# Performance work log

Measured on AMD Instinct MI355X. Metric: run time of the kernel, lower is better.

The kernel has to match this reference:

```python
import jax, jax.numpy as jnp
from jax import lax
import numpy as np

B, S, E, HID = 16, 7, 64, 64
RES = (64, 64); D = RES[0] * RES[1]
XLOW, XHIGH = -0.5, 0.5
RLOW, RHIGH = float(np.sqrt(0.01)), float(np.sqrt(0.05))
PIXEL_MULT = 1.0; N_ITER = 3; TSOFT = 1.0 / float(np.sqrt(E))

def _build_grid():
    ranges = [np.linspace(XLOW, XHIGH, r) for r in RES]
    g = np.stack(np.meshgrid(*ranges, indexing='xy'), axis=-1)
    g = g.reshape(RES[0], RES[1], -1).reshape(1, -1, 2)
    return jnp.asarray(g, dtype=jnp.float32)

ABS_GRID = _build_grid()  # [1, D, 2]

def _ln(x, g, b):
    m = jnp.mean(x, -1, keepdims=True)
    v = jnp.mean(jnp.square(x - m), -1, keepdims=True)
    return (x - m) * lax.rsqrt(v + 1e-5) * g + b

def _forward(data, slot_noise, pos_rand, conv0_w, conv0_b, conv1_w, conv1_b, conv2_w, conv2_b,
             dataN_g, dataN_b, queryN_g, queryN_b, toK_w, toK_b, toV_w, toV_b, dense_w, dense_b,
             mlp1_w, mlp1_b, mlp2_w, mlp2_b, gru_wih, gru_whh, gru_bih, gru_bhh,
             alpha1_w, alpha1_b, alpha2_w, alpha2_b, final1_w, final1_b, final2_w, final2_b,
             slots_mu, slots_logsigma):
    dn = ('NCHW', 'OIHW', 'NCHW')
    def conv(x, w, b):
        return lax.conv_general_dilated(x, w, (1, 1), 'SAME', dimension_numbers=dn) + b[None, :, None, None]
    # CNN encoder: Conv-ReLU x3, 'same' padding, k=5
    x = jax.nn.relu(conv(data, conv0_w, conv0_b))
    x = jax.nn.relu(conv(x, conv1_w, conv1_b))
    x = jax.nn.relu(conv(x, conv2_w, conv2_b))
    enc = x.transpose(0, 2, 3, 1).reshape(B, D, HID)
    enc = _ln(enc, dataN_g, dataN_b)

    queries = slots_mu + jnp.exp(slots_logsigma) * slot_noise  # [B,S,E]
    # init_slots: faithful replication (source indexes the SLOT dim, and swaps rlow/rhigh)
    pos_scale = pos_rand.at[:, :2, :].add(-0.5)
    pos_scale = pos_scale.at[:, -1, :].set((RLOW - RHIGH) * pos_rand[:, -1, :] + RHIGH)

    encK = enc @ toK_w + toK_b  # [B,D,E]
    encV = enc @ toV_w + toV_b

    def init_mlp(y):
        y = _ln(y, queryN_g, queryN_b)
        return jax.nn.relu(y @ mlp1_w + mlp1_b) @ mlp2_w + mlp2_b

    def get_kv(ps):
        # per-slot relative grid: [B,S,D,2]
        rel = (ABS_GRID[:, None] - ps[:, :, None, :2]) / ps[:, :, -1][:, :, None, None]
        eg = PIXEL_MULT * (rel @ dense_w + dense_b)  # [B,S,D,E]
        return init_mlp(encK[:, None] + eg), init_mlp(encV[:, None] + eg)

    def att_wts(q, k):
        logits = jnp.einsum('bse,bsde->bsd', q, k) * TSOFT
        att = jax.nn.softmax(logits, axis=1)  # softmax over slots
        wts = att / jnp.sum(att, -1, keepdims=True) + 1e-8
        return att, wts

    def update_frames(wts):
        new_pos = jnp.einsum('bsd,de->bse', wts, ABS_GRID[0])  # [B,S,2]
        d2 = jnp.sum(jnp.square(ABS_GRID[:, None] - new_pos[:, :, None]), -1)  # [B,S,D]
        new_scale = jnp.sqrt(jnp.einsum('bsd,bsd->bs', wts, d2))
        return jnp.concatenate([new_pos, new_scale[..., None]], -1)

    def gru(xg, h):
        gi = xg @ gru_wih.T + gru_bih
        gh = h @ gru_whh.T + gru_bhh
        ir, iz, inn = jnp.split(gi, 3, -1)
        hr, hz, hn = jnp.split(gh, 3, -1)
        r = jax.nn.sigmoid(ir + hr)
        z = jax.nn.sigmoid(iz + hz)
        n = jnp.tanh(inn + r * hn)
        return (1.0 - z) * n + z * h

    for _ in range(N_ITER):
        keys, vals = get_kv(pos_scale)
        att, wts = att_wts(_ln(queries, queryN_g, queryN_b), keys)
        pos_scale = update_frames(wts)
        upd = jnp.einsum('bsd,bsde->bse', wts, vals)
        queries = gru(upd.reshape(-1, E), queries.reshape(-1, E)).reshape(B, S, E)

    keys, _ = get_kv(pos_scale)
    att, wts = att_wts(_ln(queries, queryN_g, queryN_b), keys)
    nps = update_frames(wts)
    alpha = jax.nn.sigmoid(jax.nn.relu(queries @ alpha1_w + alpha1_b) @ alpha2_w + alpha2_b)
    slot_feat = jax.nn.relu(queries @ final1_w + final1_b) @ final2_w + final2_b + nps
    return queries, att, slot_feat, alpha

def setup_inputs() -> dict:
    ks = jax.random.split(jax.random.key(0), 20)
    f32 = jnp.float32
    def rn(i, shape, s):
        return jax.random.normal(ks[i], shape, f32) * s
    inp = dict(
        data=jax.random.normal(ks[0], (B, 1, RES[0], RES[1]), f32),
        slot_noise=jax.random.normal(ks[1], (B, S, E), f32),
        pos_rand=jax.random.uniform(ks[2], (B, S, 3), dtype=f32),
        conv0_w=rn(3, (HID, 1, 5, 5), 0.2), conv0_b=jnp.zeros(HID, f32),
        conv1_w=rn(4, (HID, HID, 5, 5), 0.025), conv1_b=jnp.zeros(HID, f32),
        conv2_w=rn(5, (HID, HID, 5, 5), 0.025), conv2_b=jnp.zeros(HID, f32),
        dataN_g=jnp.ones(HID, f32), dataN_b=jnp.zeros(HID, f32),
        queryN_g=jnp.ones(E, f32), queryN_b=jnp.zeros(E, f32),
        toK_w=rn(6, (HID, E), 0.125), toK_b=jnp.zeros(E, f32),
        toV_w=rn(7, (HID, E), 0.125), toV_b=jnp.zeros(E, f32),
        dense_w=rn(8, (2, E), 0.7), dense_b=jnp.zeros(E, f32),
        mlp1_w=rn(9, (E, E), 0.125), mlp1_b=jnp.zeros(E, f32),
        mlp2_w=rn(10, (E, E), 0.125), mlp2_b=jnp.zeros(E, f32),
        gru_wih=rn(11, (3 * E, E), 0.125), gru_whh=rn(12, (3 * E, E), 0.125),
        gru_bih=jnp.zeros(3 * E, f32), gru_bhh=jnp.zeros(3 * E, f32),
        alpha1_w=rn(13, (E, 32), 0.125), alpha1_b=jnp.zeros(32, f32),
        alpha2_w=rn(14, (32, 1), 0.18), alpha2_b=jnp.zeros(1, f32),
        final1_w=rn(15, (E, HID), 0.125), final1_b=jnp.zeros(HID, f32),
        final2_w=rn(16, (HID, 3), 0.125), final2_b=jnp.zeros(3, f32),
        slots_mu=rn(17, (1, 1, E), 1.0),
        slots_logsigma=rn(18, (1, 1, E), 0.01),
    )
    return inp

def reference(data, slot_noise, pos_rand, conv0_w, conv0_b, conv1_w, conv1_b, conv2_w, conv2_b,
              dataN_g, dataN_b, queryN_g, queryN_b, toK_w, toK_b, toV_w, toV_b, dense_w, dense_b,
              mlp1_w, mlp1_b, mlp2_w, mlp2_b, gru_wih, gru_whh, gru_bih, gru_bhh,
              alpha1_w, alpha1_b, alpha2_w, alpha2_b, final1_w, final1_b, final2_w, final2_b,
              slots_mu, slots_logsigma):
    return _forward(data, slot_noise, pos_rand, conv0_w, conv0_b, conv1_w, conv1_b, conv2_w, conv2_b,
                    dataN_g, dataN_b, queryN_g, queryN_b, toK_w, toK_b, toV_w, toV_b, dense_w, dense_b,
                    mlp1_w, mlp1_b, mlp2_w, mlp2_b, gru_wih, gru_whh, gru_bih, gru_bhh,
                    alpha1_w, alpha1_b, alpha2_w, alpha2_b, final1_w, final1_b, final2_w, final2_b,
                    slots_mu, slots_logsigma)
```

## Files before the change

kernel.cpp:

```cpp
#include <hip/hip_runtime.h>
#include <cmath>


#define RLOW_F 0.1f
#define RHIGH_F 0.22360679774997896f
#define W0CONST 1.00004096f
#define SR2 704.3386243f

typedef __attribute__((ext_vector_type(8))) __bf16 bf16x8;
typedef __attribute__((ext_vector_type(4))) float f32x4;

__device__ __forceinline__ float wsum64(float v){
  #pragma unroll
  for (int off = 32; off > 0; off >>= 1) v += __shfl_xor(v, off, 64);
  return v;
}
__device__ __forceinline__ float rdlane(float v, int l){
  return __int_as_float(__builtin_amdgcn_readlane(__float_as_int(v), l));
}
__device__ __forceinline__ unsigned short bf16bits(float v){
  __bf16 h = (__bf16)v;
  return *reinterpret_cast<unsigned short*>(&h);
}

__device__ __forceinline__ void pp_core(int row, int e, float qv,
    float px, float py, float sc,
    const float* __restrict__ qg_, const float* __restrict__ qb_,
    const float* __restrict__ dw, const float* __restrict__ db,
    const float* __restrict__ mlp2w, const float* __restrict__ mlp2b,
    float* __restrict__ absc, float* __restrict__ w2qc){
  float m = wsum64(qv) * (1.f/64.f);
  float d = qv - m;
  float var = wsum64(d*d) * (1.f/64.f);
  float qlnv = d * (1.0f/sqrtf(var + 1e-5f)) * qg_[e] + qb_[e];
  float A  = dw[e]      / sc;
  float Bv = dw[64 + e] / sc;
  absc[row*192 + e]       = A;
  absc[row*192 + 64 + e]  = Bv;
  absc[row*192 + 128 + e] = db[e] - px*A - py*Bv;
  float acc = 0.f;
  const float* wrow = mlp2w + e*64;
  for (int j = 0; j < 64; j++) acc = fmaf(wrow[j], rdlane(qlnv, j), acc);
  w2qc[row*68 + e] = acc;
  float c2 = wsum64(mlp2b[e] * qlnv);
  if (e == 0) w2qc[row*68 + 64] = c2;
}

__global__ void k_prep(const float* __restrict__ noise, const float* __restrict__ prand,
                       const float* __restrict__ mu, const float* __restrict__ logsig,
                       const float* __restrict__ qg_, const float* __restrict__ qb_,
                       const float* __restrict__ dw, const float* __restrict__ db,
                       const float* __restrict__ mlp2w, const float* __restrict__ mlp2b,
                       float* __restrict__ queries, float* __restrict__ ps,
                       float* __restrict__ absc, float* __restrict__ w2qc,
                       float* __restrict__ accF, float* __restrict__ upd){
  int row = blockIdx.x;
  int e = threadIdx.x;
  int s = row % 7;
  float qv = mu[e] + expf(logsig[e]) * noise[row*64 + e];
  queries[row*64 + e] = qv;
  upd[row*64 + e] = 0.f;
  if (e < 4) accF[row*4 + e] = 0.f;
  float pv = 0.f;
  if (e < 3){
    float pr = prand[row*3 + e];
    if (s < 2)       pv = pr - 0.5f;
    else if (s == 6) pv = (RLOW_F - RHIGH_F)*pr + RHIGH_F;
    else             pv = pr;
    ps[row*3 + e] = pv;
  }
  float px = rdlane(pv, 0), py = rdlane(pv, 1), sc = rdlane(pv, 2);
  pp_core(row, e, qv, px, py, sc, qg_, qb_, dw, db, mlp2w, mlp2b, absc, w2qc);
}

__global__ __launch_bounds__(256) void k_conv0(const float* __restrict__ in,
                        const float* __restrict__ w, const float* __restrict__ bias,
                        unsigned short* __restrict__ out){
  int bi = blockIdx.x; int b = bi >> 6; int y = bi & 63;
  int t = threadIdx.x; int lane = t & 63; int xg = t >> 6;
  __shared__ float s_in[5*68];
  __shared__ float s_w[64*25];
  __shared__ float s_out[64*65];
  for (int i = t; i < 1600; i += 256) s_w[i] = w[i];
  for (int i = t; i < 340; i += 256){
    int r = i / 68, cx = i % 68;
    int yy = y + r - 2, gx = cx - 2;
    float v = 0.f;
    if (yy >= 0 && yy < 64 && gx >= 0 && gx < 64) v = in[(b*64 + yy)*64 + gx];
    s_in[r*68 + cx] = v;
  }
  __syncthreads();
  int o = lane;
  float bvv = bias[o];
  float acc[16];
  #pragma unroll
  for (int k = 0; k < 16; k++) acc[k] = bvv;
  #pragma unroll
  for (int ky = 0; ky < 5; ky++){
    float rv[20];
    const float4* p = reinterpret_cast<const float4*>(&s_in[ky*68 + xg*16]);
    #pragma unroll
    for (int q = 0; q < 5; q++){ float4 f = p[q]; rv[q*4]=f.x; rv[q*4+1]=f.y; rv[q*4+2]=f.z; rv[q*4+3]=f.w; }
    #pragma unroll
    for (int kx = 0; kx < 5; kx++){
      float wv = s_w[o*25 + ky*5 + kx];
      #pragma unroll
      for (int k = 0; k < 16; k++) acc[k] = fmaf(rv[k+kx], wv, acc[k]);
    }
  }
  #pragma unroll
  for (int k = 0; k < 16; k++) s_out[o*65 + xg*16 + k] = fmaxf(acc[k], 0.f);
  __syncthreads();
  for (int i = t; i < 4096; i += 256){
    int px = i >> 6, ch = i & 63;
    out[((size_t)(b*64 + y)*64 + px)*64 + ch] = bf16bits(s_out[ch*65 + px]);
  }
}

__global__ void k_packconv(const float* __restrict__ w, unsigned short* __restrict__ out){
  int idx = blockIdx.x*256 + threadIdx.x;
  if (idx >= 102400) return;
  int j = idx & 7;
  int l = (idx >> 3) & 63;
  int frag = idx >> 9;
  int nt = frag & 3;
  int ks = (frag >> 2) % 10;
  int dy = frag / 40;
  int q = l >> 4, cr = l & 15;
  int k = ks*32 + q*8 + j;
  int kx = k >> 6, ch = k & 63;
  int n = nt*16 + cr;
  out[idx] = bf16bits(w[((n*64 + ch)*5 + dy)*5 + kx]);
}

__global__ __launch_bounds__(256) void k_convm(const unsigned short* __restrict__ in_bf,
                        const unsigned short* __restrict__ wpack,
                        const float* __restrict__ bias,
                        const float* __restrict__ lng, const float* __restrict__ lnb,
                        unsigned short* __restrict__ out_bf, int mode){
  int bi = blockIdx.x;
  int b = bi >> 5; int yg = (bi >> 1) & 15; int xh = bi & 1;
  int t = threadIdx.x; int wv = t >> 6; int l = t & 63;
  int q = l >> 4, cr = l & 15;
  int yr = wv >> 1, ph = wv & 1;
  int p0 = ph*16;

  __shared__ char lds[8*36*144];

  for (int ri = 0; ri < 8; ri++){
    int yy = yg*4 + ri - 2;
    bool rok = (yy >= 0 && yy < 64);
    const uint4* src = reinterpret_cast<const uint4*>(in_bf + (size_t)(b*64 + yy)*64*64);
    for (int i = t; i < 288; i += 256){
      int px = i >> 3, c8 = i & 7;
      uint4 v = {0u,0u,0u,0u};
      int gx = xh*32 + px - 2;
      if (rok && gx >= 0 && gx < 64) v = src[gx*8 + c8];
// ... 54 lines not shown
      #pragma unroll
      for (int reg = 0; reg < 4; reg++){
        int p = xh*32 + p0 + q*4 + reg;
        float v[4]; float s1 = 0.f, s2 = 0.f;
        #pragma unroll
        for (int nt = 0; nt < 4; nt++){
          v[nt] = fmaxf(acc[r][nt][reg] + bvv[nt], 0.f);
          s1 += v[nt]; s2 += v[nt]*v[nt];
        }
        #pragma unroll
        for (int m = 1; m < 16; m <<= 1){ s1 += __shfl_xor(s1, m, 64); s2 += __shfl_xor(s2, m, 64); }
        float mean = s1 * (1.f/64.f);
        float var  = s2 * (1.f/64.f) - mean*mean;
        float rstd = 1.0f/sqrtf(var + 1e-5f);
        size_t base = ((size_t)b*4096 + y*64 + p)*64;
        #pragma unroll
        for (int nt = 0; nt < 4; nt++)
          out_bf[base + nt*16 + cr] = bf16bits((v[nt] - mean)*rstd*gv[nt] + bb[nt]);
      }
    }
  }
}

__global__ void k_packw1(const float* __restrict__ w1, unsigned short* __restrict__ out){
  int idx = blockIdx.x*256 + threadIdx.x;
  int jj = idx & 7;
  int lane = (idx >> 3) & 63;
  int frag = idx >> 9;
  int ks = frag >> 2, nt = frag & 3;
  int q = lane >> 4, cr = lane & 15;
  int k = ks*32 + q*8 + jj;
  int n = nt*16 + cr;
  out[idx] = bf16bits(w1[k*64 + n]);
}

__global__ __launch_bounds__(256) void k_projm(const unsigned short* __restrict__ enc,
                       const unsigned short* __restrict__ kpack, const float* __restrict__ bk,
                       const unsigned short* __restrict__ vpack, const float* __restrict__ bvp,
                       unsigned short* __restrict__ K, unsigned short* __restrict__ V){
  int bi = blockIdx.x; int b = bi >> 6; int tile = bi & 63;
  int t = threadIdx.x; int wv = t >> 6; int l = t & 63;
  int q = l >> 4, cr = l & 15;
  int d0 = tile*64 + wv*16;

  const bf16x8* kp = reinterpret_cast<const bf16x8*>(kpack);
  const bf16x8* vp = reinterpret_cast<const bf16x8*>(vpack);
  bf16x8 KB[8], VB[8];
  #pragma unroll
  for (int f = 0; f < 8; f++){ KB[f] = kp[f*64 + l]; VB[f] = vp[f*64 + l]; }

  const unsigned short* er = enc + (size_t)(b*4096 + d0 + cr)*64;
  bf16x8 a0 = *reinterpret_cast<const bf16x8*>(er + q*8);
  bf16x8 a1 = *reinterpret_cast<const bf16x8*>(er + 32 + q*8);

  f32x4 zero = {0.f,0.f,0.f,0.f};
  f32x4 aK[4], aV[4];
  #pragma unroll
  for (int nt = 0; nt < 4; nt++){
    aK[nt] = __builtin_amdgcn_mfma_f32_16x16x32_bf16(a0, KB[nt],     zero,   0, 0, 0);
    aK[nt] = __builtin_amdgcn_mfma_f32_16x16x32_bf16(a1, KB[4 + nt], aK[nt], 0, 0, 0);
    aV[nt] = __builtin_amdgcn_mfma_f32_16x16x32_bf16(a0, VB[nt],     zero,   0, 0, 0);
    aV[nt] = __builtin_amdgcn_mfma_f32_16x16x32_bf16(a1, VB[4 + nt], aV[nt], 0, 0, 0);
  }
  #pragma unroll
  for (int nt = 0; nt < 4; nt++){
    float bkv = bk[nt*16 + cr], bvv = bvp[nt*16 + cr];
    #pragma unroll
    for (int reg = 0; reg < 4; reg++){
      size_t base = ((size_t)b*4096 + d0 + q*4 + reg)*64 + nt*16 + cr;
      K[base] = bf16bits(aK[nt][reg] + bkv);
      V[base] = bf16bits(aV[nt][reg] + bvv);
    }
  }
}

__global__ __launch_bounds__(256) void k_attnK(const unsigned short* __restrict__ encX,
     const unsigned short* __restrict__ w1pack, const float* __restrict__ mlp1b,
     const float* __restrict__ absc, const float* __restrict__ qg_,
     const float* __restrict__ qb_, const float* __restrict__ w2qc,
     float* __restrict__ att, float* __restrict__ accF){
  int bi = blockIdx.x;
  int b = bi >> 6, tile = bi & 63;
  int t = threadIdx.x; int wv = t >> 6; int l = t & 63;
  int q = l >> 4, cr = l & 15;
  int m0 = tile*64 + wv*16;
  int drow = m0 + cr;

  __shared__ float s_log[7*64];
  __shared__ float s_absc[7*192];
  __shared__ float s_wq[7*68];
  __shared__ unsigned short s_w1[4096];
  for (int i = t; i < 1344; i += 256) s_absc[i] = absc[b*7*192 + i];
  for (int i = t; i < 476;  i += 256) s_wq[i]   = w2qc[b*7*68 + i];
  {
    const uint4* g = reinterpret_cast<const uint4*>(w1pack);
    uint4* d = reinterpret_cast<uint4*>(s_w1);
    for (int i = t; i < 512; i += 256) d[i] = g[i];
  }

  const unsigned short* er = encX + (size_t)(b*4096 + drow)*64;
  float gx = -0.5f + (float)(drow & 63) * (1.f/63.f);
  float gy = -0.5f + (float)((drow >> 6) & 63) * (1.f/63.f);
  float xb[16], gq[16], bq[16];
  {
    bf16x8 ea = *reinterpret_cast<const bf16x8*>(er + q*8);
    bf16x8 eb = *reinterpret_cast<const bf16x8*>(er + 32 + q*8);
    #pragma unroll
    for (int i = 0; i < 8; i++){ xb[i] = (float)ea[i]; xb[8+i] = (float)eb[i]; }
  }
  #pragma unroll
  for (int h = 0; h < 2; h++){
    int fb = h ? (32 + q*8) : (q*8);
    const float4* g4 = reinterpret_cast<const float4*>(qg_ + fb);
    const float4* b4 = reinterpret_cast<const float4*>(qb_ + fb);
    #pragma unroll
    for (int p = 0; p < 2; p++){
      float4 gg = g4[p], bb = b4[p];
      int o = h*8 + p*4;
      gq[o+0]=gg.x; gq[o+1]=gg.y; gq[o+2]=gg.z; gq[o+3]=gg.w;
      bq[o+0]=bb.x; bq[o+1]=bb.y; bq[o+2]=bb.z; bq[o+3]=bb.w;
    }
  }
  float b1v[4];
  #pragma unroll
  for (int nt = 0; nt < 4; nt++) b1v[nt] = mlp1b[nt*16 + cr];
  __syncthreads();

  const bf16x8* wl = reinterpret_cast<const bf16x8*>(s_w1);
  f32x4 zero = {0.f, 0.f, 0.f, 0.f};

  for (int sp = 0; sp < 4; sp++){
// ... 99 lines not shown
      for (int reg = 0; reg < 4; reg++){
        s_log[s0*64 + wv*16 + q*4 + reg] = (p0[reg] + c20) * 0.125f;
        if (np == 2) s_log[sB*64 + wv*16 + q*4 + reg] = (p1[reg] + c21) * 0.125f;
      }
    }
  }
  __syncthreads();

  if (t < 64){
    float lv[7];
    #pragma unroll
    for (int s = 0; s < 7; s++) lv[s] = s_log[s*64 + t];
    float mx = lv[0];
    #pragma unroll
    for (int s = 1; s < 7; s++) mx = fmaxf(mx, lv[s]);
    float sm = 0.f;
    #pragma unroll
    for (int s = 0; s < 7; s++){ lv[s] = expf(lv[s] - mx); sm += lv[s]; }
    float inv = 1.0f / sm;
    #pragma unroll
    for (int s = 0; s < 7; s++){
      float a = lv[s] * inv;
      s_log[s*64 + t] = a;
      att[(size_t)(b*7+s)*4096 + tile*64 + t] = a;
    }
  }
  __syncthreads();

  if (t < 224){
    int s = t >> 5, r = t & 31;
    float a1 = s_log[s*64 + r];
    float a2 = s_log[s*64 + r + 32];
    float gx1 = -0.5f + (float)r * (1.f/63.f);
    float gx2 = -0.5f + (float)(r + 32) * (1.f/63.f);
    float gyc = -0.5f + (float)tile * (1.f/63.f);
    float gy2c = gyc*gyc;
    float w0 = a1 + a2;
    float w1 = a1*gx1 + a2*gx2;
    float w2 = w0*gyc;
    float w3 = a1*(gx1*gx1 + gy2c) + a2*(gx2*gx2 + gy2c);
    #pragma unroll
    for (int m = 1; m < 32; m <<= 1){
      w0 += __shfl_xor(w0, m, 64);
      w1 += __shfl_xor(w1, m, 64);
      w2 += __shfl_xor(w2, m, 64);
      w3 += __shfl_xor(w3, m, 64);
    }
    if (r == 0){
      atomicAdd(&accF[(b*7+s)*4 + 0], w0);
      atomicAdd(&accF[(b*7+s)*4 + 1], w1);
      atomicAdd(&accF[(b*7+s)*4 + 2], w2);
      atomicAdd(&accF[(b*7+s)*4 + 3], w3);
    }
  }
}

__global__ __launch_bounds__(256) void k_attnV(const unsigned short* __restrict__ encX,
     const unsigned short* __restrict__ w1pack, const float* __restrict__ mlp1b,
     const float* __restrict__ absc, const float* __restrict__ qg_,
     const float* __restrict__ qb_, const float* __restrict__ att,
     const float* __restrict__ accF, float* __restrict__ upd){
  int bi = blockIdx.x;
  int b = bi >> 6, tile = bi & 63;
  int t = threadIdx.x; int wv = t >> 6; int l = t & 63;
  int q = l >> 4, cr = l & 15;
  int m0 = tile*64 + wv*16;
  int drow = m0 + cr;

  __shared__ float s_absc[7*192];
  __shared__ float s_att[7*64];
  __shared__ float s_upd[7*64];
  __shared__ float s_inv[7];
  __shared__ unsigned short s_w1[4096];
  for (int i = t; i < 1344; i += 256) s_absc[i] = absc[b*7*192 + i];
  for (int i = t; i < 448;  i += 256){
    s_att[i] = att[(size_t)(b*7 + (i >> 6))*4096 + tile*64 + (i & 63)];
    s_upd[i] = 0.f;
  }
  if (t < 7) s_inv[t] = 1.0f / accF[(b*7 + t)*4];
  {
    const uint4* g = reinterpret_cast<const uint4*>(w1pack);
    uint4* d = reinterpret_cast<uint4*>(s_w1);
    for (int i = t; i < 512; i += 256) d[i] = g[i];
  }

  const unsigned short* er = encX + (size_t)(b*4096 + drow)*64;
  float gx = -0.5f + (float)(drow & 63) * (1.f/63.f);
  float gy = -0.5f + (float)((drow >> 6) & 63) * (1.f/63.f);
  float xb[16], gq[16], bq[16];
  {
    bf16x8 ea = *reinterpret_cast<const bf16x8*>(er + q*8);
    bf16x8 eb = *reinterpret_cast<const bf16x8*>(er + 32 + q*8);
    #pragma unroll
    for (int i = 0; i < 8; i++){ xb[i] = (float)ea[i]; xb[8+i] = (float)eb[i]; }
  }
  #pragma unroll
  for (int h = 0; h < 2; h++){
    int fb = h ? (32 + q*8) : (q*8);
    const float4* g4 = reinterpret_cast<const float4*>(qg_ + fb);
    const float4* b4 = reinterpret_cast<const float4*>(qb_ + fb);
    #pragma unroll
    for (int p = 0; p < 2; p++){
      float4 gg = g4[p], bb = b4[p];
      int o = h*8 + p*4;
      gq[o+0]=gg.x; gq[o+1]=gg.y; gq[o+2]=gg.z; gq[o+3]=gg.w;
      bq[o+0]=bb.x; bq[o+1]=bb.y; bq[o+2]=bb.z; bq[o+3]=bb.w;
    }
  }
  float b1v[4];
  #pragma unroll
  for (int nt = 0; nt < 4; nt++) b1v[nt] = mlp1b[nt*16 + cr];
  __syncthreads();

  const bf16x8* wl = reinterpret_cast<const bf16x8*>(s_w1);
  f32x4 zero = {0.f, 0.f, 0.f, 0.f};

  for (int sp = 0; sp < 4; sp++){
    int s0 = sp*2;
    int np = (sp == 3) ? 1 : 2;
    int sB = (np == 2) ? s0 + 1 : s0;
    float x0[16], x1[16];
    float s1a = 0.f, s2a = 0.f, s1b = 0.f, s2b = 0.f;
    {
      const float* Ac = s_absc + s0*192;
      #pragma unroll
      for (int h = 0; h < 2; h++){
        int fb = h ? (32 + q*8) : (q*8);
        const float4* A4 = reinterpret_cast<const float4*>(Ac + fb);
        const float4* B4 = reinterpret_cast<const float4*>(Ac + 64 + fb);
        const float4* C4 = reinterpret_cast<const float4*>(Ac + 128 + fb);
        #pragma unroll
        for (int p = 0; p < 2; p++){
          float4 Av = A4[p], Bv = B4[p], Cv = C4[p];
          int o = h*8 + p*4;
          x0[o+0] = xb[o+0] + gx*Av.x + gy*Bv.x + Cv.x;
          x0[o+1] = xb[o+1] + gx*Av.y + gy*Bv.y + Cv.y;
          x0[o+2] = xb[o+2] + gx*Av.z + gy*Bv.z + Cv.z;
          x0[o+3] = xb[o+3] + gx*Av.w + gy*Bv.w + Cv.w;
        }
      }
      #pragma unroll
      for (int k = 0; k < 16; k++){ s1a += x0[k]; s2a = fmaf(x0[k], x0[k], s2a); }
    }
    {
      const float* Ac = s_absc + sB*192;
      #pragma unroll
      for (int h = 0; h < 2; h++){
        int fb = h ? (32 + q*8) : (q*8);
        const float4* A4 = reinterpret_cast<const float4*>(Ac + fb);
        const float4* B4 = reinterpret_cast<const float4*>(Ac + 64 + fb);
        const float4* C4 = reinterpret_cast<const float4*>(Ac + 128 + fb);
        #pragma unroll
        for (int p = 0; p < 2; p++){
          float4 Av = A4[p], Bv = B4[p], Cv = C4[p];
          int o = h*8 + p*4;
          x1[o+0] = xb[o+0] + gx*Av.x + gy*Bv.x + Cv.x;
          x1[o+1] = xb[o+1] + gx*Av.y + gy*Bv.y + Cv.y;
          x1[o+2] = xb[o+2] + gx*Av.z + gy*Bv.z + Cv.z;
          x1[o+3] = xb[o+3] + gx*Av.w + gy*Bv.w + Cv.w;
        }
      }
      #pragma unroll
      for (int k = 0; k < 16; k++){ s1b += x1[k]; s2b = fmaf(x1[k], x1[k], s2b); }
    }
    s1a += __shfl_xor(s1a, 16, 64); s2a += __shfl_xor(s2a, 16, 64);
    s1b += __shfl_xor(s1b, 16, 64); s2b += __shfl_xor(s2b, 16, 64);
    s1a += __shfl_xor(s1a, 32, 64); s2a += __shfl_xor(s2a, 32, 64);
    s1b += __shfl_xor(s1b, 32, 64); s2b += __shfl_xor(s2b, 32, 64);
    float mA = s1a*(1.f/64.f);
    float rA = 1.0f/sqrtf(s2a*(1.f/64.f) - mA*mA + 1e-5f);
    float mB = s1b*(1.f/64.f);
    float rB = 1.0f/sqrtf(s2b*(1.f/64.f) - mB*mB + 1e-5f);

    bf16x8 a00, a01, a10, a11;
    #pragma unroll
    for (int k = 0; k < 8; k++){
      a00[k] = (__bf16)((x0[k]    - mA)*rA*gq[k]   + bq[k]);
      a01[k] = (__bf16)((x0[8+k]  - mA)*rA*gq[8+k] + bq[8+k]);
      a10[k] = (__bf16)((x1[k]    - mB)*rB*gq[k]   + bq[k]);
      a11[k] = (__bf16)((x1[8+k]  - mB)*rB*gq[8+k] + bq[8+k]);
    }

    f32x4 acc0[4], acc1[4];
    #pragma unroll
    for (int nt = 0; nt < 4; nt++){
      bf16x8 w0 = wl[nt*64 + l];
      bf16x8 w1f = wl[(4 + nt)*64 + l];
      acc0[nt] = __builtin_amdgcn_mfma_f32_16x16x32_bf16(a00, w0,  zero,     0, 0, 0);
      acc0[nt] = __builtin_amdgcn_mfma_f32_16x16x32_bf16(a01, w1f, acc0[nt], 0, 0, 0);
      acc1[nt] = __builtin_amdgcn_mfma_f32_16x16x32_bf16(a10, w0,  zero,     0, 0, 0);
      acc1[nt] = __builtin_amdgcn_mfma_f32_16x16x32_bf16(a11, w1f, acc1[nt], 0, 0, 0);
    }

    float rsa0 = s_inv[s0], rsa1 = s_inv[sB];
    float wr0[4], wr1[4];
    #pragma unroll
    for (int reg = 0; reg < 4; reg++){
      wr0[reg] = fmaf(s_att[s0*64 + wv*16 + q*4 + reg], rsa0, 1e-8f);
      wr1[reg] = fmaf(s_att[sB*64 + wv*16 + q*4 + reg], rsa1, 1e-8f);
    }
    float pc0[4], pc1[4];
    #pragma unroll
    for (int nt = 0; nt < 4; nt++){
      pc0[nt] = 0.f; pc1[nt] = 0.f;
      #pragma unroll
      for (int reg = 0; reg < 4; reg++){
        pc0[nt] = fmaf(wr0[reg], fmaxf(acc0[nt][reg] + b1v[nt], 0.f), pc0[nt]);
        pc1[nt] = fmaf(wr1[reg], fmaxf(acc1[nt][reg] + b1v[nt], 0.f), pc1[nt]);
      }
    }
    #pragma unroll
    for (int nt = 0; nt < 4; nt++){
      pc0[nt] += __shfl_xor(pc0[nt], 16, 64);
      pc1[nt] += __shfl_xor(pc1[nt], 16, 64);
      pc0[nt] += __shfl_xor(pc0[nt], 32, 64);
      pc1[nt] += __shfl_xor(pc1[nt], 32, 64);
    }
    if (q == 0){
      #pragma unroll
      for (int nt = 0; nt < 4; nt++){
        atomicAdd(&s_upd[s0*64 + nt*16 + cr], pc0[nt]);
        if (np == 2) atomicAdd(&s_upd[sB*64 + nt*16 + cr], pc1[nt]);
      }
    }
  }
  __syncthreads();
  for (int i = t; i < 448; i += 256)
    atomicAdd(&upd[b*448 + i], s_upd[i]);
}

__global__ void k_gru(float* __restrict__ upd, float* __restrict__ queries,
                      const float* __restrict__ wih, const float* __restrict__ whh,
                      const float* __restrict__ bih, const float* __restrict__ bhh,
                      const float* __restrict__ mlp2w, const float* __restrict__ mlp2b,
                      float* __restrict__ accF, float* __restrict__ ps,
                      const float* __restrict__ qg_, const float* __restrict__ qb_,
                      const float* __restrict__ dw, const float* __restrict__ db,
                      float* __restrict__ absc, float* __restrict__ w2qc){
  int row = blockIdx.x; int t = threadIdx.x;
  __shared__ float us[64], hs[64], xs[64], gis[192], ghs[192];
  __shared__ float s_ps3[3];
  if (t < 64){ us[t] = upd[row*64 + t]; hs[t] = queries[row*64 + t]; }
  if (t == 64){
    float sa = accF[row*4+0];
    float ax = accF[row*4+1], ay = accF[row*4+2], ar2 = accF[row*4+3];
    float isa = 1.0f/sa;
    float Wx = ax*isa, Wy = ay*isa;
    float Wg = ar2*isa + 1e-8f*SR2;
    float s2 = Wg - (Wx*Wx + Wy*Wy)*(2.f - W0CONST);
    s_ps3[0] = Wx; s_ps3[1] = Wy; s_ps3[2] = sqrtf(fmaxf(s2, 0.f));
  }
  __syncthreads();
  if (t < 64){
    float a = W0CONST * mlp2b[t];
    for (int i = 0; i < 64; i++) a = fmaf(us[i], mlp2w[i*64 + t], a);
    xs[t] = a;
  }
  __syncthreads();
  float gi = bih[t], gh = bhh[t];
  for (int e = 0; e < 64; e++){
    gi = fmaf(wih[t*64 + e], xs[e], gi);
    gh = fmaf(whh[t*64 + e], hs[e], gh);
  }
  gis[t] = gi; ghs[t] = gh;
  __syncthreads();
  if (t < 64){
    float r = 1.0f/(1.0f + expf(-(gis[t]      + ghs[t])));
    float z = 1.0f/(1.0f + expf(-(gis[64+t]   + ghs[64+t])));
    float n = tanhf(gis[128+t] + r*ghs[128+t]);
    float newq = (1.0f - z)*n + z*hs[t];
    queries[row*64 + t] = newq;
    upd[row*64 + t] = 0.f;
    if (t < 4) accF[row*4 + t] = 0.f;
    if (t < 3) ps[row*3 + t] = s_ps3[t];
    pp_core(row, t, newq, s_ps3[0], s_ps3[1], s_ps3[2],
            qg_, qb_, dw, db, mlp2w, mlp2b, absc, w2qc);
  }
}

__global__ void k_final(const float* __restrict__ queries, const float* __restrict__ accF,
                        const float* __restrict__ a1w, const float* __restrict__ a1b,
                        const float* __restrict__ a2w, const float* __restrict__ a2b,
                        const float* __restrict__ f1w, const float* __restrict__ f1b,
                        const float* __restrict__ f2w, const float* __restrict__ f2b,
                        float* __restrict__ out){
  int bs = blockIdx.x; int e = threadIdx.x;
  __shared__ float qs[64], hf[64], ha[32];
  float q = queries[bs*64 + e];
  qs[e] = q;
  out[bs*64 + e] = q;
  __syncthreads();
  float accf = f1b[e];
  for (int i = 0; i < 64; i++) accf = fmaf(qs[i], f1w[i*64 + e], accf);
  hf[e] = fmaxf(accf, 0.f);
  if (e < 32){
// ... 45 lines not shown
  const float* mlp1_w      = (const float*)d_in[19];
  const float* mlp1_b      = (const float*)d_in[20];
  const float* mlp2_w      = (const float*)d_in[21];
  const float* mlp2_b      = (const float*)d_in[22];
  const float* gru_wih     = (const float*)d_in[23];
  const float* gru_whh     = (const float*)d_in[24];
  const float* gru_bih     = (const float*)d_in[25];
  const float* gru_bhh     = (const float*)d_in[26];
  const float* alpha1_w    = (const float*)d_in[27];
  const float* alpha1_b    = (const float*)d_in[28];
  const float* alpha2_w    = (const float*)d_in[29];
  const float* alpha2_b    = (const float*)d_in[30];
  const float* final1_w    = (const float*)d_in[31];
  const float* final1_b    = (const float*)d_in[32];
  const float* final2_w    = (const float*)d_in[33];
  const float* final2_b    = (const float*)d_in[34];
  const float* slots_mu    = (const float*)d_in[35];
  const float* slots_lsig  = (const float*)d_in[36];

  float* ws   = (float*)d_ws;
  float* bufA = ws;
  float* bufB = bufA + 4194304;
  float* bufC = bufB + 4194304;
  float* attw = bufC + 4194304;
  float* queries = attw + 458752;
  float* ps   = queries + 7168;
  float* absc = ps + 512;
  float* accF = absc + 21504;
  float* upd  = accF + 512;
  float* w2qc = upd + 7168;
  unsigned short* w1pack = (unsigned short*)(w2qc + 7616);
  unsigned short* kpack  = w1pack + 4096;
  unsigned short* vpack  = kpack + 4096;
  unsigned short* wp1    = vpack + 4096;
  unsigned short* wp2    = wp1 + 102400;

  unsigned short* c0_bf = (unsigned short*)bufA;
  unsigned short* c1_bf = (unsigned short*)bufC;
  unsigned short* enc   = (unsigned short*)bufB;
  unsigned short* encK  = (unsigned short*)bufA;
  unsigned short* encV  = (unsigned short*)bufC;

  float* outq   = (float*)d_out;
  float* outatt = outq + 7168;

  k_prep<<<112, 64, 0, stream>>>(slot_noise, pos_rand, slots_mu, slots_lsig,
                                 queryN_g, queryN_b, dense_w, dense_b, mlp2_w, mlp2_b,
                                 queries, ps, absc, w2qc, accF, upd);
  k_packw1<<<16, 256, 0, stream>>>(mlp1_w, w1pack);
  k_packw1<<<16, 256, 0, stream>>>(toK_w, kpack);
  k_packw1<<<16, 256, 0, stream>>>(toV_w, vpack);
  k_packconv<<<400, 256, 0, stream>>>(conv1_w, wp1);
  k_packconv<<<400, 256, 0, stream>>>(conv2_w, wp2);
  k_conv0<<<1024, 256, 0, stream>>>(data, conv0_w, conv0_b, c0_bf);
  k_convm<<<512, 256, 0, stream>>>(c0_bf, wp1, conv1_b, nullptr, nullptr, c1_bf, 0);
  k_convm<<<512, 256, 0, stream>>>(c1_bf, wp2, conv2_b, dataN_g, dataN_b, enc, 1);
  k_projm<<<1024, 256, 0, stream>>>(enc, kpack, toK_b, vpack, toV_b, encK, encV);

  for (int p = 0; p < 4; p++){
    float* attp = (p == 3) ? outatt : attw;
    k_attnK<<<1024, 256, 0, stream>>>(encK, w1pack, mlp1_b, absc, queryN_g, queryN_b,
                                      w2qc, attp, accF);
    if (p < 3){
      k_attnV<<<1024, 256, 0, stream>>>(encV, w1pack, mlp1_b, absc, queryN_g, queryN_b,
                                        attp, accF, upd);
      k_gru<<<112, 192, 0, stream>>>(upd, queries, gru_wih, gru_whh, gru_bih, gru_bhh,
                                     mlp2_w, mlp2_b, accF, ps, queryN_g, queryN_b,
                                     dense_w, dense_b, absc, w2qc);
    }
  }
  k_final<<<112, 64, 0, stream>>>(queries, accF,
                                  alpha1_w, alpha1_b, alpha2_w, alpha2_b,
                                  final1_w, final1_b, final2_w, final2_b, outq);
}
```

Measured before the change: 522.3 us.

## Fuse attention K and V passes into one kernel and merge weight-pack launches

Folds the value-side aggregation into the attention-logit kernel. It accumulates two partial sums per slot, one weighted by the unnormalized attention and one unweighted for the epsilon term, and the GRU kernel combines them after dividing by the global attention sum. This drops the intermediate attention buffer round-trip and one launch per iteration, and all pack and prep kernels now run as a single launch. The cost is a second encV load and extra shuffles and atomics inside the fused kernel, plus a reliance on the algebraic split (a/sum + eps)·v = (a·v)/sum + eps·v being accurate enough.

```diff
diff --git a/kernel.cpp b/kernel.cpp
--- a/kernel.cpp
+++ b/kernel.cpp
@@ -46,31 +46,70 @@
   if (e == 0) w2qc[row*68 + 64] = c2;
 }
 
-__global__ void k_prep(const float* __restrict__ noise, const float* __restrict__ prand,
-                       const float* __restrict__ mu, const float* __restrict__ logsig,
-                       const float* __restrict__ qg_, const float* __restrict__ qb_,
-                       const float* __restrict__ dw, const float* __restrict__ db,
-                       const float* __restrict__ mlp2w, const float* __restrict__ mlp2b,
-                       float* __restrict__ queries, float* __restrict__ ps,
-                       float* __restrict__ absc, float* __restrict__ w2qc,
-                       float* __restrict__ accF, float* __restrict__ upd){
-  int row = blockIdx.x;
-  int e = threadIdx.x;
-  int s = row % 7;
-  float qv = mu[e] + expf(logsig[e]) * noise[row*64 + e];
-  queries[row*64 + e] = qv;
-  upd[row*64 + e] = 0.f;
-  if (e < 4) accF[row*4 + e] = 0.f;
-  float pv = 0.f;
-  if (e < 3){
-    float pr = prand[row*3 + e];
-    if (s < 2)       pv = pr - 0.5f;
-    else if (s == 6) pv = (RLOW_F - RHIGH_F)*pr + RHIGH_F;
-    else             pv = pr;
-    ps[row*3 + e] = pv;
-  }
-  float px = rdlane(pv, 0), py = rdlane(pv, 1), sc = rdlane(pv, 2);
-  pp_core(row, e, qv, px, py, sc, qg_, qb_, dw, db, mlp2w, mlp2b, absc, w2qc);
+__global__ void k_packall(const float* __restrict__ mlp1_w, const float* __restrict__ toK_w,
+                          const float* __restrict__ toV_w, const float* __restrict__ conv1_w,
+                          const float* __restrict__ conv2_w,
+                          unsigned short* __restrict__ w1pack, unsigned short* __restrict__ kpack,
+                          unsigned short* __restrict__ vpack, unsigned short* __restrict__ wp1,
+                          unsigned short* __restrict__ wp2,
+                          const float* __restrict__ noise, const float* __restrict__ prand,
+                          const float* __restrict__ mu, const float* __restrict__ logsig,
+                          const float* __restrict__ qg_, const float* __restrict__ qb_,
+                          const float* __restrict__ dw, const float* __restrict__ db,
+                          const float* __restrict__ mlp2w, const float* __restrict__ mlp2b,
+                          float* __restrict__ queries, float* __restrict__ ps,
+                          float* __restrict__ absc, float* __restrict__ w2qc,
+                          float* __restrict__ accF, float* __restrict__ upd){
+  int bi = blockIdx.x; int t = threadIdx.x;
+  if (bi < 48){
+    const float* src = (bi < 16) ? mlp1_w : ((bi < 32) ? toK_w : toV_w);
+    unsigned short* dst = (bi < 16) ? w1pack : ((bi < 32) ? kpack : vpack);
+    int idx = (bi & 15)*256 + t;
+    int jj = idx & 7;
+    int lane = (idx >> 3) & 63;
+    int frag = idx >> 9;
+    int ks = frag >> 2, nt = frag & 3;
+    int q = lane >> 4, cr = lane & 15;
+    int k = ks*32 + q*8 + jj;
+    int n = nt*16 + cr;
+    dst[idx] = bf16bits(src[k*64 + n]);
+  } else if (bi < 848){
+    int rb = bi - 48;
+    const float* src = (rb < 400) ? conv1_w : conv2_w;
+    unsigned short* dst = (rb < 400) ? wp1 : wp2;
+    int idx = (rb % 400)*256 + t;
+    int j = idx & 7;
+    int l = (idx >> 3) & 63;
+    int frag = idx >> 9;
+    int nt = frag & 3;
+    int ks = (frag >> 2) % 10;
+    int dy = frag / 40;
+    int q = l >> 4, cr = l & 15;
+    int k = ks*32 + q*8 + j;
+    int kx = k >> 6, ch = k & 63;
+    int n = nt*16 + cr;
+    dst[idx] = bf16bits(src[((n*64 + ch)*5 + dy)*5 + kx]);
+  } else {
+    if (t >= 64) return;
+    int row = bi - 848;
+    int e = t;
+    int s = row % 7;
+    float qv = mu[e] + expf(logsig[e]) * noise[row*64 + e];
+    queries[row*64 + e] = qv;
+    upd[row*128 + e] = 0.f;
+    upd[row*128 + 64 + e] = 0.f;
+    if (e < 4) accF[row*4 + e] = 0.f;
+    float pv = 0.f;
+    if (e < 3){
+      float pr = prand[row*3 + e];
+      if (s < 2)       pv = pr - 0.5f;
+      else if (s == 6) pv = (RLOW_F - RHIGH_F)*pr + RHIGH_F;
+      else             pv = pr;
+      ps[row*3 + e] = pv;
+    }
+    float px = rdlane(pv, 0), py = rdlane(pv, 1), sc = rdlane(pv, 2);
+    pp_core(row, e, qv, px, py, sc, qg_, qb_, dw, db, mlp2w, mlp2b, absc, w2qc);
+  }
 }
 
 __global__ __launch_bounds__(256) void k_conv0(const float* __restrict__ in,
@@ -117,22 +156,6 @@
   }
 }
 
-__global__ void k_packconv(const float* __restrict__ w, unsigned short* __restrict__ out){
-  int idx = blockIdx.x*256 + threadIdx.x;
-  if (idx >= 102400) return;
-  int j = idx & 7;
-  int l = (idx >> 3) & 63;
-  int frag = idx >> 9;
-  int nt = frag & 3;
-  int ks = (frag >> 2) % 10;
-  int dy = frag / 40;
-  int q = l >> 4, cr = l & 15;
-  int k = ks*32 + q*8 + j;
-  int kx = k >> 6, ch = k & 63;
-  int n = nt*16 + cr;
-  out[idx] = bf16bits(w[((n*64 + ch)*5 + dy)*5 + kx]);
-}
-
 __global__ __launch_bounds__(256) void k_convm(const unsigned short* __restrict__ in_bf,
                         const unsigned short* __restrict__ wpack,
                         const float* __restrict__ bias,
@@ -233,18 +256,6 @@
   }
 }
 
-__global__ void k_packw1(const float* __restrict__ w1, unsigned short* __restrict__ out){
-  int idx = blockIdx.x*256 + threadIdx.x;
-  int jj = idx & 7;
-  int lane = (idx >> 3) & 63;
-  int frag = idx >> 9;
-  int ks = frag >> 2, nt = frag & 3;
-  int q = lane >> 4, cr = lane & 15;
-  int k = ks*32 + q*8 + jj;
-  int n = nt*16 + cr;
-  out[idx] = bf16bits(w1[k*64 + n]);
-}
-
 __global__ __launch_bounds__(256) void k_projm(const unsigned short* __restrict__ enc,
                        const unsigned short* __restrict__ kpack, const float* __restrict__ bk,
                        const unsigned short* __restrict__ vpack, const float* __restrict__ bvp,
@@ -285,11 +296,13 @@
   }
 }
 
-__global__ __launch_bounds__(256) void k_attnK(const unsigned short* __restrict__ encX,
+__global__ __launch_bounds__(256) void k_attn(const unsigned short* __restrict__ encK,
+     const unsigned short* __restrict__ encV,
      const unsigned short* __restrict__ w1pack, const float* __restrict__ mlp1b,
      const float* __restrict__ absc, const float* __restrict__ qg_,
      const float* __restrict__ qb_, const float* __restrict__ w2qc,
-     float* __restrict__ att, float* __restrict__ accF){
+     float* __restrict__ attOut, float* __restrict__ accF,
+     float* __restrict__ upd, int mode){
   int bi = blockIdx.x;
   int b = bi >> 6, tile = bi & 63;
   int t = threadIdx.x; int wv = t >> 6; int l = t & 63;
@@ -300,16 +313,19 @@
   __shared__ float s_log[7*64];
   __shared__ float s_absc[7*192];
   __shared__ float s_wq[7*68];
+  __shared__ float s_upd[7*128];
   __shared__ unsigned short s_w1[4096];
   for (int i = t; i < 1344; i += 256) s_absc[i] = absc[b*7*192 + i];
   for (int i = t; i < 476;  i += 256) s_wq[i]   = w2qc[b*7*68 + i];
+  if (mode == 0)
+    for (int i = t; i < 896; i += 256) s_upd[i] = 0.f;
   {
     const uint4* g = reinterpret_cast<const uint4*>(w1pack);
     uint4* d = reinterpret_cast<uint4*>(s_w1);
     for (int i = t; i < 512; i += 256) d[i] = g[i];
   }
 
-  const unsigned short* er = encX + (size_t)(b*4096 + drow)*64;
+  const unsigned short* er = encK + (size_t)(b*4096 + drow)*64;
   float gx = -0.5f + (float)(drow & 63) * (1.f/63.f);
   float gy = -0.5f + (float)((drow >> 6) & 63) * (1.f/63.f);
   float xb[16], gq[16], bq[16];
@@ -318,6 +334,12 @@
     bf16x8 eb = *reinterpret_cast<const bf16x8*>(er + 32 + q*8);
     #pragma unroll
     for (int i = 0; i < 8; i++){ xb[i] = (float)ea[i]; xb[8+i] = (float)eb[i]; }
+  }
+  bf16x8 vb0, vb1;
+  if (mode == 0){
+    const unsigned short* ev = encV + (size_t)(b*4096 + drow)*64;
+    vb0 = *reinterpret_cast<const bf16x8*>(ev + q*8);
+    vb1 = *reinterpret_cast<const bf16x8*>(ev + 32 + q*8);
   }
   #pragma unroll
   for (int h = 0; h < 2; h++){
@@ -463,7 +485,7 @@
     for (int s = 0; s < 7; s++){
       float a = lv[s] * inv;
       s_log[s*64 + t] = a;
-      att[(size_t)(b*7+s)*4096 + tile*64 + t] = a;
+      if (mode == 1) attOut[(size_t)(b*7+s)*4096 + tile*64 + t] = a;
     }
   }
   __syncthreads();
@@ -494,180 +516,129 @@
       atomicAdd(&accF[(b*7+s)*4 + 3], w3);
     }
   }
-}
-
-__global__ __launch_bounds__(256) void k_attnV(const unsigned short* __restrict__ encX,
-     const unsigned short* __restrict__ w1pack, const float* __restrict__ mlp1b,
-     const float* __restrict__ absc, const float* __restrict__ qg_,
-     const float* __restrict__ qb_, const float* __restrict__ att,
-     const float* __restrict__ accF, float* __restrict__ upd){
-  int bi = blockIdx.x;
-  int b = bi >> 6, tile = bi & 63;
-  int t = threadIdx.x; int wv = t >> 6; int l = t & 63;
-  int q = l >> 4, cr = l & 15;
-  int m0 = tile*64 + wv*16;
-  int drow = m0 + cr;
-
-  __shared__ float s_absc[7*192];
-  __shared__ float s_att[7*64];
-  __shared__ float s_upd[7*64];
-  __shared__ float s_inv[7];
-  __shared__ unsigned short s_w1[4096];
-  for (int i = t; i < 1344; i += 256) s_absc[i] = absc[b*7*192 + i];
-  for (int i = t; i < 448;  i += 256){
-    s_att[i] = att[(size_t)(b*7 + (i >> 6))*4096 + tile*64 + (i & 63)];
-    s_upd[i] = 0.f;
-  }
-  if (t < 7) s_inv[t] = 1.0f / accF[(b*7 + t)*4];
-  {
-    const uint4* g = reinterpret_cast<const uint4*>(w1pack);
-    uint4* d = reinterpret_cast<uint4*>(s_w1);
-    for (int i = t; i < 512; i += 256) d[i] = g[i];
-  }
-
-  const unsigned short* er = encX + (size_t)(b*4096 + drow)*64;
-  float gx = -0.5f + (float)(drow & 63) * (1.f/63.f);
-  float gy = -0.5f + (float)((drow >> 6) & 63) * (1.f/63.f);
-  float xb[16], gq[16], bq[16];
-  {
-    bf16x8 ea = *reinterpret_cast<const bf16x8*>(er + q*8);
-    bf16x8 eb = *reinterpret_cast<const bf16x8*>(er + 32 + q*8);
-    #pragma unroll
-    for (int i = 0; i < 8; i++){ xb[i] = (float)ea[i]; xb[8+i] = (float)eb[i]; }
-  }
-  #pragma unroll
-  for (int h = 0; h < 2; h++){
-    int fb = h ? (32 + q*8) : (q*8);
-    const float4* g4 = reinterpret_cast<const float4*>(qg_ + fb);
-    const float4* b4 = reinterpret_cast<const float4*>(qb_ + fb);
-    #pragma unroll
-    for (int p = 0; p < 2; p++){
-      float4 gg = g4[p], bb = b4[p];
-      int o = h*8 + p*4;
-      gq[o+0]=gg.x; gq[o+1]=gg.y; gq[o+2]=gg.z; gq[o+3]=gg.w;
-      bq[o+0]=bb.x; bq[o+1]=bb.y; bq[o+2]=bb.z; bq[o+3]=bb.w;
-    }
-  }
-  float b1v[4];
-  #pragma unroll
-  for (int nt = 0; nt < 4; nt++) b1v[nt] = mlp1b[nt*16 + cr];
-  __syncthreads();
-
-  const bf16x8* wl = reinterpret_cast<const bf16x8*>(s_w1);
-  f32x4 zero = {0.f, 0.f, 0.f, 0.f};
-
-  for (int sp = 0; sp < 4; sp++){
-    int s0 = sp*2;
-    int np = (sp == 3) ? 1 : 2;
-    int sB = (np == 2) ? s0 + 1 : s0;
-    float x0[16], x1[16];
-    float s1a = 0.f, s2a = 0.f, s1b = 0.f, s2b = 0.f;
-    {
-      const float* Ac = s_absc + s0*192;
-      #pragma unroll
-      for (int h = 0; h < 2; h++){
-        int fb = h ? (32 + q*8) : (q*8);
-        const float4* A4 = reinterpret_cast<const float4*>(Ac + fb);
-        const float4* B4 = reinterpret_cast<const float4*>(Ac + 64 + fb);
-        const float4* C4 = reinterpret_cast<const float4*>(Ac + 128 + fb);
-        #pragma unroll
-        for (int p = 0; p < 2; p++){
-          float4 Av = A4[p], Bv = B4[p], Cv = C4[p];
-          int o = h*8 + p*4;
-          x0[o+0] = xb[o+0] + gx*Av.x + gy*Bv.x + Cv.x;
-          x0[o+1] = xb[o+1] + gx*Av.y + gy*Bv.y + Cv.y;
-          x0[o+2] = xb[o+2] + gx*Av.z + gy*Bv.z + Cv.z;
-          x0[o+3] = xb[o+3] + gx*Av.w + gy*Bv.w + Cv.w;
+
+  if (mode == 0){
+    float xbv[16];
+    #pragma unroll
+    for (int i = 0; i < 8; i++){ xbv[i] = (float)vb0[i]; xbv[8+i] = (float)vb1[i]; }
+    for (int sp = 0; sp < 4; sp++){
+      int s0 = sp*2;
+      int np = (sp == 3) ? 1 : 2;
+      int sB = (np == 2) ? s0 + 1 : s0;
+      float x0[16], x1[16];
+      float s1a = 0.f, s2a = 0.f, s1b = 0.f, s2b = 0.f;
+      {
+        const float* Ac = s_absc + s0*192;
+        #pragma unroll
+        for (int h = 0; h < 2; h++){
+          int fb = h ? (32 + q*8) : (q*8);
+          const float4* A4 = reinterpret_cast<const float4*>(Ac + fb);
+          const float4* B4 = reinterpret_cast<const float4*>(Ac + 64 + fb);
+          const float4* C4 = reinterpret_cast<const float4*>(Ac + 128 + fb);
+          #pragma unroll
+          for (int p = 0; p < 2; p++){
+            float4 Av = A4[p], Bv = B4[p], Cv = C4[p];
+            int o = h*8 + p*4;
+            x0[o+0] = xbv[o+0] + gx*Av.x + gy*Bv.x + Cv.x;
+            x0[o+1] = xbv[o+1] + gx*Av.y + gy*Bv.y + Cv.y;
+            x0[o+2] = xbv[o+2] + gx*Av.z + gy*Bv.z + Cv.z;
+            x0[o+3] = xbv[o+3] + gx*Av.w + gy*Bv.w + Cv.w;
+          }
         }
-      }
-      #pragma unroll
-      for (int k = 0; k < 16; k++){ s1a += x0[k]; s2a = fmaf(x0[k], x0[k], s2a); }
-    }
-    {
-      const float* Ac = s_absc + sB*192;
-      #pragma unroll
-      for (int h = 0; h < 2; h++){
-        int fb = h ? (32 + q*8) : (q*8);
-        const float4* A4 = reinterpret_cast<const float4*>(Ac + fb);
-        const float4* B4 = reinterpret_cast<const float4*>(Ac + 64 + fb);
-        const float4* C4 = reinterpret_cast<const float4*>(Ac + 128 + fb);
-        #pragma unroll
-        for (int p = 0; p < 2; p++){
-          float4 Av = A4[p], Bv = B4[p], Cv = C4[p];
-          int o = h*8 + p*4;
-          x1[o+0] = xb[o+0] + gx*Av.x + gy*Bv.x + Cv.x;
-          x1[o+1] = xb[o+1] + gx*Av.y + gy*Bv.y + Cv.y;
-          x1[o+2] = xb[o+2] + gx*Av.z + gy*Bv.z + Cv.z;
-          x1[o+3] = xb[o+3] + gx*Av.w + gy*Bv.w + Cv.w;
+        #pragma unroll
+        for (int k = 0; k < 16; k++){ s1a += x0[k]; s2a = fmaf(x0[k], x0[k], s2a); }
+      }
+      {
+        const float* Ac = s_absc + sB*192;
+        #pragma unroll
+        for (int h = 0; h < 2; h++){
+          int fb = h ? (32 + q*8) : (q*8);
+          const float4* A4 = reinterpret_cast<const float4*>(Ac + fb);
+          const float4* B4 = reinterpret_cast<const float4*>(Ac + 64 + fb);
+          const float4* C4 = reinterpret_cast<const float4*>(Ac + 128 + fb);
+          #pragma unroll
+          for (int p = 0; p < 2; p++){
+            float4 Av = A4[p], Bv = B4[p], Cv = C4[p];
+            int o = h*8 + p*4;
+            x1[o+0] = xbv[o+0] + gx*Av.x + gy*Bv.x + Cv.x;
+            x1[o+1] = xbv[o+1] + gx*Av.y + gy*Bv.y + Cv.y;
+            x1[o+2] = xbv[o+2] + gx*Av.z + gy*Bv.z + Cv.z;
+            x1[o+3] = xbv[o+3] + gx*Av.w + gy*Bv.w + Cv.w;
+          }
         }
-      }
-      #pragma unroll
-      for (int k = 0; k < 16; k++){ s1b += x1[k]; s2b = fmaf(x1[k], x1[k], s2b); }
-    }
-    s1a += __shfl_xor(s1a, 16, 64); s2a += __shfl_xor(s2a, 16, 64);
-    s1b += __shfl_xor(s1b, 16, 64); s2b += __shfl_xor(s2b, 16, 64);
-    s1a += __shfl_xor(s1a, 32, 64); s2a += __shfl_xor(s2a, 32, 64);
-    s1b += __shfl_xor(s1b, 32, 64); s2b += __shfl_xor(s2b, 32, 64);
-    float mA = s1a*(1.f/64.f);
-    float rA = 1.0f/sqrtf(s2a*(1.f/64.f) - mA*mA + 1e-5f);
-    float mB = s1b*(1.f/64.f);
-    float rB = 1.0f/sqrtf(s2b*(1.f/64.f) - mB*mB + 1e-5f);
-
-    bf16x8 a00, a01, a10, a11;
-    #pragma unroll
-    for (int k = 0; k < 8; k++){
-      a00[k] = (__bf16)((x0[k]    - mA)*rA*gq[k]   + bq[k]);
-      a01[k] = (__bf16)((x0[8+k]  - mA)*rA*gq[8+k] + bq[8+k]);
-      a10[k] = (__bf16)((x1[k]    - mB)*rB*gq[k]   + bq[k]);
-      a11[k] = (__bf16)((x1[8+k]  - mB)*rB*gq[8+k] + bq[8+k]);
-    }
-
-    f32x4 acc0[4], acc1[4];
-    #pragma unroll
-    for (int nt = 0; nt < 4; nt++){
-      bf16x8 w0 = wl[nt*64 + l];
-      bf16x8 w1f = wl[(4 + nt)*64 + l];
-      acc0[nt] = __builtin_amdgcn_mfma_f32_16x16x32_bf16(a00, w0,  zero,     0, 0, 0);
-      acc0[nt] = __builtin_amdgcn_mfma_f32_16x16x32_bf16(a01, w1f, acc0[nt], 0, 0, 0);
-      acc1[nt] = __builtin_amdgcn_mfma_f32_16x16x32_bf16(a10, w0,  zero,     0, 0, 0);
-      acc1[nt] = __builtin_amdgcn_mfma_f32_16x16x32_bf16(a11, w1f, acc1[nt], 0, 0, 0);
-    }
-
-    float rsa0 = s_inv[s0], rsa1 = s_inv[sB];
-    float wr0[4], wr1[4];
-    #pragma unroll
-    for (int reg = 0; reg < 4; reg++){
-      wr0[reg] = fmaf(s_att[s0*64 + wv*16 + q*4 + reg], rsa0, 1e-8f);
-      wr1[reg] = fmaf(s_att[sB*64 + wv*16 + q*4 + reg], rsa1, 1e-8f);
-    }
-    float pc0[4], pc1[4];
-    #pragma unroll
-    for (int nt = 0; nt < 4; nt++){
-      pc0[nt] = 0.f; pc1[nt] = 0.f;
+        #pragma unroll
+        for (int k = 0; k < 16; k++){ s1b += x1[k]; s2b = fmaf(x1[k], x1[k], s2b); }
+      }
+      s1a += __shfl_xor(s1a, 16, 64); s2a += __shfl_xor(s2a, 16, 64);
+      s1b += __shfl_xor(s1b, 16, 64); s2b += __shfl_xor(s2b, 16, 64);
+      s1a += __shfl_xor(s1a, 32, 64); s2a += __shfl_xor(s2a, 32, 64);
+      s1b += __shfl_xor(s1b, 32, 64); s2b += __shfl_xor(s2b, 32, 64);
+      float mA = s1a*(1.f/64.f);
+      float rA = 1.0f/sqrtf(s2a*(1.f/64.f) - mA*mA + 1e-5f);
+      float mB = s1b*(1.f/64.f);
+      float rB = 1.0f/sqrtf(s2b*(1.f/64.f) - mB*mB + 1e-5f);
+
+      bf16x8 a00, a01, a10, a11;
+      #pragma unroll
+      for (int k = 0; k < 8; k++){
+        a00[k] = (__bf16)((x0[k]    - mA)*rA*gq[k]   + bq[k]);
+        a01[k] = (__bf16)((x0[8+k]  - mA)*rA*gq[8+k] + bq[8+k]);
+        a10[k] = (__bf16)((x1[k]    - mB)*rB*gq[k]   + bq[k]);
+        a11[k] = (__bf16)((x1[8+k]  - mB)*rB*gq[8+k] + bq[8+k]);
+      }
+
+      f32x4 acc0[4], acc1[4];
+      #pragma unroll
+      for (int nt = 0; nt < 4; nt++){
+        bf16x8 w0 = wl[nt*64 + l];
+        bf16x8 w1f = wl[(4 + nt)*64 + l];
+        acc0[nt] = __builtin_amdgcn_mfma_f32_16x16x32_bf16(a00, w0,  zero,     0, 0, 0);
+        acc0[nt] = __builtin_amdgcn_mfma_f32_16x16x32_bf16(a01, w1f, acc0[nt], 0, 0, 0);
+        acc1[nt] = __builtin_amdgcn_mfma_f32_16x16x32_bf16(a10, w0,  zero,     0, 0, 0);
+        acc1[nt] = __builtin_amdgcn_mfma_f32_16x16x32_bf16(a11, w1f, acc1[nt], 0, 0, 0);
+      }
+
+      float wr0[4], wr1[4];
       #pragma unroll
       for (int reg = 0; reg < 4; reg++){
-        pc0[nt] = fmaf(wr0[reg], fmaxf(acc0[nt][reg] + b1v[nt], 0.f), pc0[nt]);
-        pc1[nt] = fmaf(wr1[reg], fmaxf(acc1[nt][reg] + b1v[nt], 0.f), pc1[nt]);
-      }
-    }
-    #pragma unroll
-    for (int nt = 0; nt < 4; nt++){
-      pc0[nt] += __shfl_xor(pc0[nt], 16, 64);
-      pc1[nt] += __shfl_xor(pc1[nt], 16, 64);
-      pc0[nt] += __shfl_xor(pc0[nt], 32, 64);
-      pc1[nt] += __shfl_xor(pc1[nt], 32, 64);
-    }
-    if (q == 0){
+        wr0[reg] = s_log[s0*64 + wv*16 + q*4 + reg];
+        wr1[reg] = s_log[sB*64 + wv*16 + q*4 + reg];
+      }
+      float pa0[4], pa1[4], pu0[4], pu1[4];
       #pragma unroll
       for (int nt = 0; nt < 4; nt++){
-        atomicAdd(&s_upd[s0*64 + nt*16 + cr], pc0[nt]);
-        if (np == 2) atomicAdd(&s_upd[sB*64 + nt*16 + cr], pc1[nt]);
-      }
-    }
-  }
-  __syncthreads();
-  for (int i = t; i < 448; i += 256)
-    atomicAdd(&upd[b*448 + i], s_upd[i]);
+        pa0[nt] = 0.f; pa1[nt] = 0.f; pu0[nt] = 0.f; pu1[nt] = 0.f;
+        #pragma unroll
+        for (int reg = 0; reg < 4; reg++){
+          float v0 = fmaxf(acc0[nt][reg] + b1v[nt], 0.f);
+          float v1 = fmaxf(acc1[nt][reg] + b1v[nt], 0.f);
+          pa0[nt] = fmaf(wr0[reg], v0, pa0[nt]); pu0[nt] += v0;
+          pa1[nt] = fmaf(wr1[reg], v1, pa1[nt]); pu1[nt] += v1;
+        }
+      }
+      #pragma unroll
+      for (int nt = 0; nt < 4; nt++){
+        pa0[nt] += __shfl_xor(pa0[nt], 16, 64); pa0[nt] += __shfl_xor(pa0[nt], 32, 64);
+        pu0[nt] += __shfl_xor(pu0[nt], 16, 64); pu0[nt] += __shfl_xor(pu0[nt], 32, 64);
+        pa1[nt] += __shfl_xor(pa1[nt], 16, 64); pa1[nt] += __shfl_xor(pa1[nt], 32, 64);
+        pu1[nt] += __shfl_xor(pu1[nt], 16, 64); pu1[nt] += __shfl_xor(pu1[nt], 32, 64);
+      }
+      if (q == 0){
+        #pragma unroll
+        for (int nt = 0; nt < 4; nt++){
+          atomicAdd(&s_upd[s0*128 + nt*16 + cr], pa0[nt]);
+          atomicAdd(&s_upd[s0*128 + 64 + nt*16 + cr], pu0[nt]);
+          if (np == 2){
+            atomicAdd(&s_upd[sB*128 + nt*16 + cr], pa1[nt]);
+            atomicAdd(&s_upd[sB*128 + 64 + nt*16 + cr], pu1[nt]);
+          }
+        }
+      }
+    }
+    __syncthreads();
+    for (int i = t; i < 896; i += 256)
+      atomicAdd(&upd[b*896 + i], s_upd[i]);
+  }
 }
 
 __global__ void k_gru(float* __restrict__ upd, float* __restrict__ queries,
@@ -681,7 +652,11 @@
   int row = blockIdx.x; int t = threadIdx.x;
   __shared__ float us[64], hs[64], xs[64], gis[192], ghs[192];
   __shared__ float s_ps3[3];
-  if (t < 64){ us[t] = upd[row*64 + t]; hs[t] = queries[row*64 + t]; }
+  if (t < 64){
+    float isa0 = 1.0f/accF[row*4];
+    us[t] = upd[row*128 + t]*isa0 + 1e-8f*upd[row*128 + 64 + t];
+    hs[t] = queries[row*64 + t];
+  }
   if (t == 64){
     float sa = accF[row*4+0];
     float ax = accF[row*4+1], ay = accF[row*4+2], ar2 = accF[row*4+3];
@@ -711,7 +686,8 @@
     float n = tanhf(gis[128+t] + r*ghs[128+t]);
     float newq = (1.0f - z)*n + z*hs[t];
     queries[row*64 + t] = newq;
-    upd[row*64 + t] = 0.f;
+    upd[row*128 + t] = 0.f;
+    upd[row*128 + 64 + t] = 0.f;
     if (t < 4) accF[row*4 + t] = 0.f;
     if (t < 3) ps[row*3 + t] = s_ps3[t];
     pp_core(row, t, newq, s_ps3[0], s_ps3[1], s_ps3[2],
@@ -803,13 +779,12 @@
   float* bufA = ws;
   float* bufB = bufA + 4194304;
   float* bufC = bufB + 4194304;
-  float* attw = bufC + 4194304;
-  float* queries = attw + 458752;
+  float* queries = bufC + 4194304;
   float* ps   = queries + 7168;
   float* absc = ps + 512;
   float* accF = absc + 21504;
   float* upd  = accF + 512;
-  float* w2qc = upd + 7168;
+  float* w2qc = upd + 14336;
   unsigned short* w1pack = (unsigned short*)(w2qc + 7616);
   unsigned short* kpack  = w1pack + 4096;
   unsigned short* vpack  = kpack + 4096;
@@ -825,26 +800,21 @@
   float* outq   = (float*)d_out;
   float* outatt = outq + 7168;
 
-  k_prep<<<112, 64, 0, stream>>>(slot_noise, pos_rand, slots_mu, slots_lsig,
-                                 queryN_g, queryN_b, dense_w, dense_b, mlp2_w, mlp2_b,
-                                 queries, ps, absc, w2qc, accF, upd);
-  k_packw1<<<16, 256, 0, stream>>>(mlp1_w, w1pack);
-  k_packw1<<<16, 256, 0, stream>>>(toK_w, kpack);
-  k_packw1<<<16, 256, 0, stream>>>(toV_w, vpack);
-  k_packconv<<<400, 256, 0, stream>>>(conv1_w, wp1);
-  k_packconv<<<400, 256, 0, stream>>>(conv2_w, wp2);
+  k_packall<<<960, 256, 0, stream>>>(mlp1_w, toK_w, toV_w, conv1_w, conv2_w,
+                                     w1pack, kpack, vpack, wp1, wp2,
+                                     slot_noise, pos_rand, slots_mu, slots_lsig,
+                                     queryN_g, queryN_b, dense_w, dense_b, mlp2_w, mlp2_b,
+                                     queries, ps, absc, w2qc, accF, upd);
   k_conv0<<<1024, 256, 0, stream>>>(data, conv0_w, conv0_b, c0_bf);
   k_convm<<<512, 256, 0, stream>>>(c0_bf, wp1, conv1_b, nullptr, nullptr, c1_bf, 0);
   k_convm<<<512, 256, 0, stream>>>(c1_bf, wp2, conv2_b, dataN_g, dataN_b, enc, 1);
   k_projm<<<1024, 256, 0, stream>>>(enc, kpack, toK_b, vpack, toV_b, encK, encV);
 
   for (int p = 0; p < 4; p++){
-    float* attp = (p == 3) ? outatt : attw;
-    k_attnK<<<1024, 256, 0, stream>>>(encK, w1pack, mlp1_b, absc, queryN_g, queryN_b,
-                                      w2qc, attp, accF);
+    k_attn<<<1024, 256, 0, stream>>>(encK, encV, w1pack, mlp1_b, absc,
+                                     queryN_g, queryN_b, w2qc, outatt, accF, upd,
+                                     (p < 3) ? 0 : 1);
     if (p < 3){
-      k_attnV<<<1024, 256, 0, stream>>>(encV, w1pack, mlp1_b, absc, queryN_g, queryN_b,
-                                        attp, accF, upd);
       k_gru<<<112, 192, 0, stream>>>(upd, queries, gru_wih, gru_whh, gru_bih, gru_bhh,
                                      mlp2_w, mlp2_b, accF, ps, queryN_g, queryN_b,
                                      dense_w, dense_b, absc, w2qc);
```

After: 486.6 us. -6.8%, faster.
